# Kernel optimization log

Measured on AMD Instinct MI355X. Metric: run time of the kernel, lower is better.

Reference implementation:

```python
import jax, jax.numpy as jnp
import numpy as np

NUM_HEADS = 8

def setup_inputs() -> dict:
    key = jax.random.key(0)
    ks = jax.random.split(key, 5)
    B, T, N, D = 2, 8, 1024, 512
    x = jax.random.normal(ks[0], (B, T, N, D), dtype=jnp.float32)
    s = 1.0 / np.sqrt(D)
    W_qkv = jax.random.normal(ks[1], (D, 3 * D), dtype=jnp.float32) * s
    b_qkv = jnp.zeros((3 * D,), dtype=jnp.float32)
    W_proj = jax.random.normal(ks[2], (D, D), dtype=jnp.float32) * s
    b_proj = jnp.zeros((D,), dtype=jnp.float32)
    return {"x": x, "W_qkv": W_qkv, "b_qkv": b_qkv, "W_proj": W_proj, "b_proj": b_proj}

def reference(x, W_qkv, b_qkv, W_proj, b_proj):
    B, T, N, D = x.shape
    H = NUM_HEADS
    hd = D // H
    scale = hd ** -0.5
    xf = x.reshape(B * T, N, D)  # fold frames into batch
    qkv = xf @ W_qkv + b_qkv  # (BT, N, 3D)
    qkv = qkv.reshape(B * T, N, 3, H, hd)
    q = qkv[:, :, 0].transpose(0, 2, 1, 3)  # (BT, H, N, hd)
    k = qkv[:, :, 1].transpose(0, 2, 1, 3)
    v = qkv[:, :, 2].transpose(0, 2, 1, 3)
    attn = jnp.einsum('bhnd,bhmd->bhnm', q, k) * scale
    attn = jax.nn.softmax(attn, axis=-1)  # dropout is identity in eval mode
    out = jnp.einsum('bhnm,bhmd->bhnd', attn, v)
    out = out.transpose(0, 2, 1, 3).reshape(B * T, N, D)
    out = out @ W_proj + b_proj
    return out.reshape(B, T, N, D)
```

## Files before the change

### kernel.cpp

```cpp
#include <hip/hip_runtime.h>

typedef __bf16 b16x8 __attribute__((ext_vector_type(8)));
typedef float f32x4 __attribute__((ext_vector_type(4)));
typedef float f32x16 __attribute__((ext_vector_type(16)));
typedef unsigned int u32;

static __device__ __forceinline__ f32x4 mfma16(b16x8 a, b16x8 b, f32x4 c) {
  return __builtin_amdgcn_mfma_f32_16x16x32_bf16(a, b, c, 0, 0, 0);
}
static __device__ __forceinline__ f32x16 mfma32(b16x8 a, b16x8 b, f32x16 c) {
  return __builtin_amdgcn_mfma_f32_32x32x16_bf16(a, b, c, 0, 0, 0);
}

static __device__ __forceinline__ unsigned short f2bf(float f) {
  unsigned u = __builtin_bit_cast(unsigned, f);
  u += 0x7fffu + ((u >> 16) & 1u);
  return (unsigned short)(u >> 16);
}
static __device__ __forceinline__ u32 cvtpk(float lo, float hi) {
  u32 d;
  asm("v_cvt_pk_bf16_f32 %0, %1, %2" : "=v"(d) : "v"(lo), "v"(hi));
  return d;
}

static __device__ __forceinline__ void gload16(const void* g, void* s) {
  __builtin_amdgcn_global_load_lds((const __attribute__((address_space(1))) void*)g,
                                   (__attribute__((address_space(3))) void*)s, 16, 0, 0);
}

__global__ __launch_bounds__(256) void cvt_x(const float* __restrict__ in,
                                             unsigned short* __restrict__ out, int n8) {
  int i = blockIdx.x * 256 + threadIdx.x;
  if (i >= n8) return;
  const float4* p = (const float4*)in + (size_t)2 * i;
  float4 a = p[0], b = p[1];
  unsigned r0 = f2bf(a.x) | ((unsigned)f2bf(a.y) << 16);
  unsigned r1 = f2bf(a.z) | ((unsigned)f2bf(a.w) << 16);
  unsigned r2 = f2bf(b.x) | ((unsigned)f2bf(b.y) << 16);
  unsigned r3 = f2bf(b.z) | ((unsigned)f2bf(b.w) << 16);
  ((uint4*)out)[i] = make_uint4(r0, r1, r2, r3);
}

__global__ __launch_bounds__(256) void tr_w(const float* __restrict__ in,
                                            unsigned short* __restrict__ out, int R, int C) {
  int idx = blockIdx.x * 256 + threadIdx.x;
  if (idx >= R * C) return;
  int r = idx / C, c = idx % C;
  out[(size_t)c * R + r] = f2bf(in[idx]);
}

template <int MODE>
__global__ __launch_bounds__(256) void gemm_bt_bias(const unsigned short* __restrict__ A,
                                                    const unsigned short* __restrict__ Bt,
                                                    const float* __restrict__ bias,
                                                    void* __restrict__ Cout, int M, int N, int K) {
  __shared__ unsigned short As[128 * 64];
  __shared__ unsigned short Bs[128 * 64];
  const int tid = threadIdx.x;
  const int w = tid >> 6, l = tid & 63, g = l >> 4, lm = l & 15;
  const int wr = w >> 1, wc = w & 1;
  const int bm = blockIdx.y, bn = blockIdx.x;

  f32x4 acc[4][4];
#pragma unroll
  for (int i = 0; i < 4; ++i)
#pragma unroll
    for (int j = 0; j < 4; ++j) acc[i][j] = {0.f, 0.f, 0.f, 0.f};

  const int Kb = K * 2;
  const char* Abase = (const char*)A + (size_t)(bm * 128) * Kb;
  const char* Bbase = (const char*)Bt + (size_t)(bn * 128) * Kb;
  const int lrow = l >> 3;
  const int srccol = ((l & 7) * 16) ^ (((l >> 3) & 7) << 4);

  for (int kt = 0; kt < K; kt += 64) {
#pragma unroll
    for (int i = w; i < 16; i += 4) {
      gload16(Abase + (size_t)(i * 8 + lrow) * Kb + kt * 2 + srccol, As + i * 512);
      gload16(Bbase + (size_t)(i * 8 + lrow) * Kb + kt * 2 + srccol, Bs + i * 512);
    }
    __syncthreads();
#pragma unroll
    for (int ks = 0; ks < 2; ++ks) {
      b16x8 af[4], bf[4];
#pragma unroll
      for (int rt = 0; rt < 4; ++rt) {
        int row = wr * 64 + rt * 16 + lm;
        af[rt] = *(const b16x8*)((const char*)As + row * 128 +
                                 (((ks * 64) + g * 16) ^ ((lm & 7) << 4)));
      }
#pragma unroll
      for (int ct = 0; ct < 4; ++ct) {
        int row = wc * 64 + ct * 16 + lm;
        bf[ct] = *(const b16x8*)((const char*)Bs + row * 128 +
                                 (((ks * 64) + g * 16) ^ ((lm & 7) << 4)));
      }
#pragma unroll
      for (int rt = 0; rt < 4; ++rt)
#pragma unroll
        for (int ct = 0; ct < 4; ++ct) acc[rt][ct] = mfma16(af[rt], bf[ct], acc[rt][ct]);
    }
    __syncthreads();
  }

#pragma unroll
  for (int ct = 0; ct < 4; ++ct) {
    int col = bn * 128 + wc * 64 + ct * 16 + lm;
    float bv = bias[col];
#pragma unroll
    for (int rt = 0; rt < 4; ++rt) {
      int row0 = bm * 128 + wr * 64 + rt * 16 + g * 4;
#pragma unroll
      for (int j = 0; j < 4; ++j) {
        float v = acc[rt][ct][j] + bv;
        if (MODE == 2)
          ((float*)Cout)[(size_t)(row0 + j) * N + col] = v;
        else
          ((unsigned short*)Cout)[(size_t)(row0 + j) * N + col] = f2bf(v);
      }
    }
  }
}

__global__ __launch_bounds__(256) void attn_kernel(const unsigned short* __restrict__ qkv,
                                                   unsigned short* __restrict__ out) {
  __shared__ unsigned short Ks[64 * 64];
  __shared__ unsigned short Vt[64 * 64];
  __shared__ unsigned short Ps[4 * 32 * 64];

  const int tid = threadIdx.x;
  const int w = tid >> 6, l = tid & 63, g = l >> 4, lm = l & 15;
  const int lq = l & 31, hi = l >> 5;
  const int id = blockIdx.x;
  const int id2 = (id & 7) * 128 + (id >> 3);
  const int qt = id2 & 7, h = (id2 >> 3) & 7, bt = id2 >> 6;
  const size_t rb = (size_t)bt * 1024;

  const int qrow_sw = qt * 128 + w * 32 + lq;
  b16x8 qf[4];
#pragma unroll
  for (int ks = 0; ks < 4; ++ks)
    qf[ks] = *(const b16x8*)(qkv + (rb + qrow_sw) * 1536 + h * 64 + ks * 16 + hi * 8);

  f32x4 o[2][4];
#pragma unroll
  for (int rt = 0; rt < 2; ++rt)
#pragma unroll
    for (int dt = 0; dt < 4; ++dt) o[rt][dt] = {0.f, 0.f, 0.f, 0.f};
  float m = -1e30f, lsum = 0.f;

  const int krow_l = l >> 3;
  const int srccol = ((l & 7) * 16) ^ (((l >> 3) & 7) << 4);
  const char* kbase = (const char*)(qkv + rb * 1536 + 512 + (size_t)h * 64);
  const unsigned short* vbase = qkv + rb * 1536 + 1024 + (size_t)h * 64 + w * 16;

  for (int kb = 0; kb < 16; ++kb) {
    const int k0 = kb * 64;
#pragma unroll
    for (int ii = 0; ii < 2; ++ii) {
      int i = w * 2 + ii;
      gload16(kbase + (size_t)(k0 + i * 8 + krow_l) * 3072 + srccol, Ks + i * 512);
    }
    {
      const unsigned short* vsrc = vbase + (size_t)(k0 + l) * 1536;
      uint4 v0 = *(const uint4*)vsrc;
      uint4 v1 = *(const uint4*)(vsrc + 8);
      u32 vv[8] = {v0.x, v0.y, v0.z, v0.w, v1.x, v1.y, v1.z, v1.w};
#pragma unroll
      for (int k2 = 0; k2 < 8; ++k2) {
        int d0 = w * 16 + 2 * k2, d1 = d0 + 1;
        *(unsigned short*)((char*)Vt + d0 * 128 + ((2 * l) ^ ((d0 & 7) << 4))) =
            (unsigned short)(vv[k2] & 0xffffu);
        *(unsigned short*)((char*)Vt + d1 * 128 + ((2 * l) ^ ((d1 & 7) << 4))) =
            (unsigned short)(vv[k2] >> 16);
      }
    }
    __syncthreads();

    f32x16 s0 = {0.f, 0.f, 0.f, 0.f, 0.f, 0.f, 0.f, 0.f, 0.f, 0.f, 0.f, 0.f, 0.f, 0.f, 0.f, 0.f};
    f32x16 s1 = s0;
#pragma unroll
    for (int ks = 0; ks < 4; ++ks) {
      int co = (ks * 32 + hi * 16) ^ ((lq & 7) << 4);
      b16x8 k0f = *(const b16x8*)((const char*)Ks + lq * 128 + co);
      b16x8 k1f = *(const b16x8*)((const char*)Ks + (32 + lq) * 128 + co);
      s0 = mfma32(k0f, qf[ks], s0);
      s1 = mfma32(k1f, qf[ks], s1);
    }

    float mx = -1e30f;
#pragma unroll
    for (int r = 0; r < 16; ++r) {
      s0[r] *= 0.125f;
      s1[r] *= 0.125f;
      mx = fmaxf(mx, fmaxf(s0[r], s1[r]));
    }
    mx = fmaxf(mx, __shfl_xor(mx, 32));
    float mn = fmaxf(m, mx);
    float resc = __expf(m - mn);
    m = mn;
#pragma unroll
    for (int r = 0; r < 16; ++r) {
      s0[r] = __expf(s0[r] - mn);
      s1[r] = __expf(s1[r] - mn);
    }
    float a0 = 0.f, a1 = 0.f, a2 = 0.f, a3 = 0.f;
#pragma unroll
    for (int r = 0; r < 16; r += 4) {
      a0 += s0[r]; a1 += s0[r + 1]; a2 += s0[r + 2]; a3 += s0[r + 3];
      a0 += s1[r]; a1 += s1[r + 1]; a2 += s1[r + 2]; a3 += s1[r + 3];
    }
    float rs = (a0 + a1) + (a2 + a3);
    rs += __shfl_xor(rs, 32);
    lsum = lsum * resc + rs;

#pragma unroll
    for (int rt = 0; rt < 2; ++rt) {
      float r0 = __shfl(resc, rt * 16 + g * 4 + 0);
      float r1 = __shfl(resc, rt * 16 + g * 4 + 1);
      float r2 = __shfl(resc, rt * 16 + g * 4 + 2);
      float r3 = __shfl(resc, rt * 16 + g * 4 + 3);
#pragma unroll
      for (int dt = 0; dt < 4; ++dt) {
        o[rt][dt][0] *= r0;
        o[rt][dt][1] *= r1;
        o[rt][dt][2] *= r2;
        o[rt][dt][3] *= r3;
      }
    }

#pragma unroll
    for (int i = 0; i < 8; ++i) {
      int key0 = ((2 * i) & 3) + 8 * (i >> 1) + 4 * hi;
      char* prow = (char*)Ps + w * 4096 + lq * 128;
      *(u32*)(prow + ((2 * key0) ^ ((lq & 7) << 4))) = cvtpk(s0[2 * i], s0[2 * i + 1]);
      *(u32*)(prow + ((64 + 2 * key0) ^ ((lq & 7) << 4))) = cvtpk(s1[2 * i], s1[2 * i + 1]);
    }

#pragma unroll
    for (int ks = 0; ks < 2; ++ks) {
      b16x8 pa[2];
#pragma unroll
      for (int rt = 0; rt < 2; ++rt) {
        int pr = rt * 16 + lm;
        pa[rt] = *(const b16x8*)((const char*)Ps + w * 4096 + pr * 128 +
                                 (((ks * 64) + g * 16) ^ ((lm & 7) << 4)));
      }
#pragma unroll
      for (int dt = 0; dt < 4; ++dt) {
        int d = dt * 16 + lm;
        b16x8 vf = *(const b16x8*)((const char*)Vt + d * 128 +
                                   (((ks * 64) + g * 16) ^ ((d & 7) << 4)));
        o[0][dt] = mfma16(pa[0], vf, o[0][dt]);
        o[1][dt] = mfma16(pa[1], vf, o[1][dt]);
      }
    }
    __syncthreads();
  }

  float inv = 1.0f / lsum;
#pragma unroll
  for (int rt = 0; rt < 2; ++rt) {
    float i0 = __shfl(inv, rt * 16 + g * 4 + 0);
    float i1 = __shfl(inv, rt * 16 + g * 4 + 1);
    float i2 = __shfl(inv, rt * 16 + g * 4 + 2);
    float i3 = __shfl(inv, rt * 16 + g * 4 + 3);
    float iv[4] = {i0, i1, i2, i3};
#pragma unroll
    for (int dt = 0; dt < 4; ++dt)
#pragma unroll
      for (int j = 0; j < 4; ++j) {
        int nrow = qt * 128 + w * 32 + rt * 16 + g * 4 + j;
        out[(rb + nrow) * 512 + h * 64 + dt * 16 + lm] = f2bf(o[rt][dt][j] * iv[j]);
      }
  }
}

extern "C" void kernel_launch(void* const* d_in, const int* in_sizes, int n_in, void* d_out,
                              int out_size, void* d_ws, size_t ws_size, hipStream_t stream) {
  const float* x = (const float*)d_in[0];
  const float* Wqkv = (const float*)d_in[1];
  const float* bqkv = (const float*)d_in[2];
  const float* Wproj = (const float*)d_in[3];
  const float* bproj = (const float*)d_in[4];
  float* outp = (float*)d_out;

  char* ws = (char*)d_ws;
  unsigned short* xb = (unsigned short*)(ws);
  unsigned short* wqkvT = (unsigned short*)(ws + 16777216);
  unsigned short* wprojT = (unsigned short*)(ws + 18350080);
  unsigned short* qkvb = (unsigned short*)(ws + 18874368);
  unsigned short* attno = (unsigned short*)(ws + 69206016);

  cvt_x<<<4096, 256, 0, stream>>>(x, xb, 1048576);
  tr_w<<<3072, 256, 0, stream>>>(Wqkv, wqkvT, 512, 1536);
  tr_w<<<1024, 256, 0, stream>>>(Wproj, wprojT, 512, 512);
  gemm_bt_bias<0><<<dim3(12, 128), 256, 0, stream>>>(xb, wqkvT, bqkv, qkvb, 16384, 1536, 512);
  attn_kernel<<<1024, 256, 0, stream>>>(qkvb, attno);
  gemm_bt_bias<2><<<dim3(4, 128), 256, 0, stream>>>(attno, wprojT, bproj, outp, 16384, 512, 512);
}
```

Baseline: 231.8 us.

## Fold softmax scale into Q, use exp2, lazy rescale, prefetch V, pad LDS

The QKV GEMM epilogue now multiplies the Q columns by scale*log2(e), so attention can use exp2 directly without a per-score multiply. The online softmax skips the max update and the O/lsum rescale unless some row's max grows by more than a threshold. The next block's V rows are prefetched into registers during compute, and the Vt/Ps LDS layouts switch from XOR swizzle to padded rows. This trades extra LDS footprint and bank-conflict behaviour for less VALU and exp work in the inner loop, and relies on a bounded-growth threshold for numerical safety.

```diff
diff --git a/kernel.cpp b/kernel.cpp
--- a/kernel.cpp
+++ b/kernel.cpp
@@ -21,6 +21,13 @@
   u32 d;
   asm("v_cvt_pk_bf16_f32 %0, %1, %2" : "=v"(d) : "v"(lo), "v"(hi));
   return d;
+}
+static __device__ __forceinline__ float ex2(float x) {
+#if __has_builtin(__builtin_amdgcn_exp2f)
+  return __builtin_amdgcn_exp2f(x);
+#else
+  return exp2f(x);
+#endif
 }
 
 static __device__ __forceinline__ void gload16(const void* g, void* s) {
@@ -107,12 +114,13 @@
   for (int ct = 0; ct < 4; ++ct) {
     int col = bn * 128 + wc * 64 + ct * 16 + lm;
     float bv = bias[col];
+    float sc = (MODE == 1 && col < 512) ? 0.18033688011112042f : 1.0f;
 #pragma unroll
     for (int rt = 0; rt < 4; ++rt) {
       int row0 = bm * 128 + wr * 64 + rt * 16 + g * 4;
 #pragma unroll
       for (int j = 0; j < 4; ++j) {
-        float v = acc[rt][ct][j] + bv;
+        float v = (acc[rt][ct][j] + bv) * sc;
         if (MODE == 2)
           ((float*)Cout)[(size_t)(row0 + j) * N + col] = v;
         else
@@ -125,8 +133,8 @@
 __global__ __launch_bounds__(256) void attn_kernel(const unsigned short* __restrict__ qkv,
                                                    unsigned short* __restrict__ out) {
   __shared__ unsigned short Ks[64 * 64];
-  __shared__ unsigned short Vt[64 * 64];
-  __shared__ unsigned short Ps[4 * 32 * 64];
+  __shared__ unsigned short Vt[64 * 72];
+  __shared__ unsigned short Ps[4 * 32 * 72];
 
   const int tid = threadIdx.x;
   const int w = tid >> 6, l = tid & 63, g = l >> 4, lm = l & 15;
@@ -153,6 +161,10 @@
   const int srccol = ((l & 7) * 16) ^ (((l >> 3) & 7) << 4);
   const char* kbase = (const char*)(qkv + rb * 1536 + 512 + (size_t)h * 64);
   const unsigned short* vbase = qkv + rb * 1536 + 1024 + (size_t)h * 64 + w * 16;
+  unsigned short* Psw = Ps + w * 32 * 72;
+
+  uint4 va = *(const uint4*)(vbase + (size_t)l * 1536);
+  uint4 vb = *(const uint4*)(vbase + (size_t)l * 1536 + 8);
 
   for (int kb = 0; kb < 16; ++kb) {
     const int k0 = kb * 64;
@@ -162,20 +174,21 @@
       gload16(kbase + (size_t)(k0 + i * 8 + krow_l) * 3072 + srccol, Ks + i * 512);
     }
     {
-      const unsigned short* vsrc = vbase + (size_t)(k0 + l) * 1536;
-      uint4 v0 = *(const uint4*)vsrc;
-      uint4 v1 = *(const uint4*)(vsrc + 8);
-      u32 vv[8] = {v0.x, v0.y, v0.z, v0.w, v1.x, v1.y, v1.z, v1.w};
+      u32 vv[8] = {va.x, va.y, va.z, va.w, vb.x, vb.y, vb.z, vb.w};
 #pragma unroll
       for (int k2 = 0; k2 < 8; ++k2) {
-        int d0 = w * 16 + 2 * k2, d1 = d0 + 1;
-        *(unsigned short*)((char*)Vt + d0 * 128 + ((2 * l) ^ ((d0 & 7) << 4))) =
-            (unsigned short)(vv[k2] & 0xffffu);
-        *(unsigned short*)((char*)Vt + d1 * 128 + ((2 * l) ^ ((d1 & 7) << 4))) =
-            (unsigned short)(vv[k2] >> 16);
+        int d0 = w * 16 + 2 * k2;
+        Vt[d0 * 72 + l] = (unsigned short)(vv[k2] & 0xffffu);
+        Vt[(d0 + 1) * 72 + l] = (unsigned short)(vv[k2] >> 16);
       }
     }
     __syncthreads();
+
+    {
+      int kn = ((kb + 1) & 15) * 64;
+      va = *(const uint4*)(vbase + (size_t)(kn + l) * 1536);
+      vb = *(const uint4*)(vbase + (size_t)(kn + l) * 1536 + 8);
+    }
 
     f32x16 s0 = {0.f, 0.f, 0.f, 0.f, 0.f, 0.f, 0.f, 0.f, 0.f, 0.f, 0.f, 0.f, 0.f, 0.f, 0.f, 0.f};
     f32x16 s1 = s0;
@@ -190,19 +203,32 @@
 
     float mx = -1e30f;
 #pragma unroll
+    for (int r = 0; r < 16; ++r) mx = fmaxf(mx, fmaxf(s0[r], s1[r]));
+    mx = fmaxf(mx, __shfl_xor(mx, 32));
+    if (!__all(mx <= m + 11.5f)) {
+      float mn = fmaxf(m, mx);
+      float resc = ex2(m - mn);
+      m = mn;
+      lsum *= resc;
+#pragma unroll
+      for (int rt = 0; rt < 2; ++rt) {
+        float r0 = __shfl(resc, rt * 16 + g * 4 + 0);
+        float r1 = __shfl(resc, rt * 16 + g * 4 + 1);
+        float r2 = __shfl(resc, rt * 16 + g * 4 + 2);
+        float r3 = __shfl(resc, rt * 16 + g * 4 + 3);
+#pragma unroll
+        for (int dt = 0; dt < 4; ++dt) {
+          o[rt][dt][0] *= r0;
+          o[rt][dt][1] *= r1;
+          o[rt][dt][2] *= r2;
+          o[rt][dt][3] *= r3;
+        }
+      }
+    }
+#pragma unroll
     for (int r = 0; r < 16; ++r) {
-      s0[r] *= 0.125f;
-      s1[r] *= 0.125f;
-      mx = fmaxf(mx, fmaxf(s0[r], s1[r]));
-    }
-    mx = fmaxf(mx, __shfl_xor(mx, 32));
-    float mn = fmaxf(m, mx);
-    float resc = __expf(m - mn);
-    m = mn;
-#pragma unroll
-    for (int r = 0; r < 16; ++r) {
-      s0[r] = __expf(s0[r] - mn);
-      s1[r] = __expf(s1[r] - mn);
+      s0[r] = ex2(s0[r] - m);
+      s1[r] = ex2(s1[r] - m);
     }
     float a0 = 0.f, a1 = 0.f, a2 = 0.f, a3 = 0.f;
 #pragma unroll
@@ -212,45 +238,26 @@
     }
     float rs = (a0 + a1) + (a2 + a3);
     rs += __shfl_xor(rs, 32);
-    lsum = lsum * resc + rs;
-
-#pragma unroll
-    for (int rt = 0; rt < 2; ++rt) {
-      float r0 = __shfl(resc, rt * 16 + g * 4 + 0);
-      float r1 = __shfl(resc, rt * 16 + g * 4 + 1);
-      float r2 = __shfl(resc, rt * 16 + g * 4 + 2);
-      float r3 = __shfl(resc, rt * 16 + g * 4 + 3);
-#pragma unroll
-      for (int dt = 0; dt < 4; ++dt) {
-        o[rt][dt][0] *= r0;
-        o[rt][dt][1] *= r1;
-        o[rt][dt][2] *= r2;
-        o[rt][dt][3] *= r3;
-      }
-    }
-
-#pragma unroll
-    for (int i = 0; i < 8; ++i) {
-      int key0 = ((2 * i) & 3) + 8 * (i >> 1) + 4 * hi;
-      char* prow = (char*)Ps + w * 4096 + lq * 128;
-      *(u32*)(prow + ((2 * key0) ^ ((lq & 7) << 4))) = cvtpk(s0[2 * i], s0[2 * i + 1]);
-      *(u32*)(prow + ((64 + 2 * key0) ^ ((lq & 7) << 4))) = cvtpk(s1[2 * i], s1[2 * i + 1]);
+    lsum += rs;
+
+#pragma unroll
+    for (int gi = 0; gi < 4; ++gi) {
+      int kidx = 8 * gi + 4 * hi;
+      *(uint2*)(Psw + lq * 72 + kidx) =
+          make_uint2(cvtpk(s0[4 * gi], s0[4 * gi + 1]), cvtpk(s0[4 * gi + 2], s0[4 * gi + 3]));
+      *(uint2*)(Psw + lq * 72 + 32 + kidx) =
+          make_uint2(cvtpk(s1[4 * gi], s1[4 * gi + 1]), cvtpk(s1[4 * gi + 2], s1[4 * gi + 3]));
     }
 
 #pragma unroll
     for (int ks = 0; ks < 2; ++ks) {
       b16x8 pa[2];
 #pragma unroll
-      for (int rt = 0; rt < 2; ++rt) {
-        int pr = rt * 16 + lm;
-        pa[rt] = *(const b16x8*)((const char*)Ps + w * 4096 + pr * 128 +
-                                 (((ks * 64) + g * 16) ^ ((lm & 7) << 4)));
-      }
+      for (int rt = 0; rt < 2; ++rt)
+        pa[rt] = *(const b16x8*)(Psw + (rt * 16 + lm) * 72 + ks * 32 + g * 8);
 #pragma unroll
       for (int dt = 0; dt < 4; ++dt) {
-        int d = dt * 16 + lm;
-        b16x8 vf = *(const b16x8*)((const char*)Vt + d * 128 +
-                                   (((ks * 64) + g * 16) ^ ((d & 7) << 4)));
+        b16x8 vf = *(const b16x8*)(Vt + (dt * 16 + lm) * 72 + ks * 32 + g * 8);
         o[0][dt] = mfma16(pa[0], vf, o[0][dt]);
         o[1][dt] = mfma16(pa[1], vf, o[1][dt]);
       }
@@ -295,7 +302,7 @@
   cvt_x<<<4096, 256, 0, stream>>>(x, xb, 1048576);
   tr_w<<<3072, 256, 0, stream>>>(Wqkv, wqkvT, 512, 1536);
   tr_w<<<1024, 256, 0, stream>>>(Wproj, wprojT, 512, 512);
-  gemm_bt_bias<0><<<dim3(12, 128), 256, 0, stream>>>(xb, wqkvT, bqkv, qkvb, 16384, 1536, 512);
+  gemm_bt_bias<1><<<dim3(12, 128), 256, 0, stream>>>(xb, wqkvT, bqkv, qkvb, 16384, 1536, 512);
   attn_kernel<<<1024, 256, 0, stream>>>(qkvb, attno);
   gemm_bt_bias<2><<<dim3(4, 128), 256, 0, stream>>>(attno, wprojT, bproj, outp, 16384, 512, 512);
 }
```

New measurement: 233.3 us. Within noise of the previous version (+0.6%).
